# Optimization experiments

Measured on AMD Instinct MI355X. Metric: run time of the kernel, lower is better.

Reference implementation:

```python
import jax, jax.numpy as jnp
import numpy as np


def setup_inputs() -> dict:
    key = jax.random.key(0)
    k1, k2, k3, k4 = jax.random.split(key, 4)
    B, C, T, H, W = 2, 64, 8, 48, 48
    C2 = C // 2
    x_in = jax.random.normal(k1, (B, C, T, H, W), dtype=jnp.float32)
    # per-time-slice 1x1 conv weights (theta/phi pairs), kaiming-ish scale
    theta_w = jax.random.normal(k2, (T, C2, C), dtype=jnp.float32) / np.sqrt(C)
    phi_w = jax.random.normal(k3, (T, C2, C), dtype=jnp.float32) / np.sqrt(C)
    out_w = jax.random.normal(k4, (C, C), dtype=jnp.float32) / np.sqrt(C)
    return {"x_in": x_in, "theta_w": theta_w, "phi_w": phi_w, "out_w": out_w}


def reference(x_in, theta_w, phi_w, out_w):
    B, C, T, H, W = x_in.shape
    C2 = theta_w.shape[1]
    P = H * W
    # [B, T, C, P] layout: flatten spatial, move time next to batch
    x = jnp.transpose(x_in, (0, 2, 1, 3, 4)).reshape(B, T, C, P)
    # per-slice 1x1 convs == per-slice channel matmuls with slice-specific weights
    theta = jnp.einsum("toc,btcp->btop", theta_w, x)  # [B,T,C2,P]
    phi = jnp.einsum("toc,btcp->btop", phi_w, x)      # [B,T,C2,P]
    scale = 1.0 / jnp.sqrt(jnp.asarray(C2, dtype=x_in.dtype))
    scores = jnp.einsum("btcp,btcq->btpq", theta, phi) * scale  # [B,T,P,P]
    attn = jax.nn.softmax(scores, axis=-1)
    f = jnp.einsum("btpq,btcq->btcp", attn, x)  # value = raw x, [B,T,C,P]
    # conv_out: 1x1x1 Conv3d (pointwise over channels), then residual
    out = jnp.einsum("oc,btcp->btop", out_w, f)
    out = jnp.transpose(out.reshape(B, T, C, H, W), (0, 2, 1, 3, 4))
    return out + x_in
```

## Files before the change

kernel.cpp:

```cpp
#include <hip/hip_runtime.h>
#include <hip/hip_bf16.h>

#define CC 64
#define TT 8
#define PP 2304
#define C2 32
#define BT 16
#define NKT 36
#define QKT 9
#define SCALE2 0.25503486f

using h8 = __attribute__((ext_vector_type(8))) _Float16;
using h4 = __attribute__((ext_vector_type(4))) _Float16;
using f4 = __attribute__((ext_vector_type(4))) float;

#if __has_builtin(__builtin_amdgcn_exp2f)
#define EXP2(v) __builtin_amdgcn_exp2f(v)
#else
#define EXP2(v) exp2f(v)
#endif

#define SWIZ_BT(xcd, g) ((xcd) + 8 * ((g) & 1))


__global__ __launch_bounds__(256) void k_prep(
    const float* __restrict__ x, const float* __restrict__ tw,
    const float* __restrict__ pw, _Float16* __restrict__ thf,
    _Float16* __restrict__ rec) {
  const int qt = blockIdx.y >> 1, bt = SWIZ_BT(blockIdx.x, blockIdx.y);
  const int b = bt >> 3, t = bt & 7;
  const int tid = threadIdx.x;
  const int wv = tid >> 6, lane = tid & 63;
  const int quad = lane >> 4, l15 = lane & 15;

  __shared__ __align__(16) float x_s[64][68];
  __shared__ __align__(16) _Float16 th_s[4][16][32];
  __shared__ __align__(16) _Float16 ph_s[4][16][32];

  const size_t xslice = ((size_t)b * CC * TT + t) * PP;
  const int qg0 = qt * 64;

  {
    const int l16 = tid & 15;
    const int crow = tid >> 4;
#pragma unroll
    for (int ppass = 0; ppass < 4; ppass++) {
      const int c = ppass * 16 + crow;
      float4 u = *reinterpret_cast<const float4*>(
          &x[xslice + (size_t)c * (TT * PP) + qg0 + l16 * 4]);
      x_s[l16 * 4 + 0][c] = u.x;
      x_s[l16 * 4 + 1][c] = u.y;
      x_s[l16 * 4 + 2][c] = u.z;
      x_s[l16 * 4 + 3][c] = u.w;
    }
  }
  __syncthreads();

  h8 bx[2];
#pragma unroll
  for (int ks = 0; ks < 2; ks++) {
    const float* row = &x_s[wv * 16 + l15][ks * 32 + quad * 8];
    float4 u0 = *reinterpret_cast<const float4*>(row);
    float4 u1 = *reinterpret_cast<const float4*>(row + 4);
    bx[ks][0] = (_Float16)u0.x; bx[ks][1] = (_Float16)u0.y;
    bx[ks][2] = (_Float16)u0.z; bx[ks][3] = (_Float16)u0.w;
    bx[ks][4] = (_Float16)u1.x; bx[ks][5] = (_Float16)u1.y;
    bx[ks][6] = (_Float16)u1.z; bx[ks][7] = (_Float16)u1.w;
  }

  const float* twt = tw + t * C2 * CC;
  const float* pwt = pw + t * C2 * CC;
  const f4 zero = {0.f, 0.f, 0.f, 0.f};
  f4 accT[2] = {zero, zero}, accP[2] = {zero, zero};
#pragma unroll
  for (int mt = 0; mt < 2; mt++)
#pragma unroll
    for (int ks = 0; ks < 2; ks++) {
      const float* wr = twt + (mt * 16 + l15) * CC + ks * 32 + quad * 8;
      const float* pr = pwt + (mt * 16 + l15) * CC + ks * 32 + quad * 8;
      float4 a0 = *reinterpret_cast<const float4*>(wr);
      float4 a1 = *reinterpret_cast<const float4*>(wr + 4);
      float4 p0 = *reinterpret_cast<const float4*>(pr);
      float4 p1 = *reinterpret_cast<const float4*>(pr + 4);
      h8 at = {(_Float16)a0.x, (_Float16)a0.y, (_Float16)a0.z, (_Float16)a0.w,
               (_Float16)a1.x, (_Float16)a1.y, (_Float16)a1.z, (_Float16)a1.w};
      h8 ap = {(_Float16)p0.x, (_Float16)p0.y, (_Float16)p0.z, (_Float16)p0.w,
               (_Float16)p1.x, (_Float16)p1.y, (_Float16)p1.z, (_Float16)p1.w};
      accT[mt] =
          __builtin_amdgcn_mfma_f32_16x16x32_f16(at, bx[ks], accT[mt], 0, 0, 0);
      accP[mt] =
          __builtin_amdgcn_mfma_f32_16x16x32_f16(ap, bx[ks], accP[mt], 0, 0, 0);
    }

#pragma unroll
  for (int mt = 0; mt < 2; mt++) {
    h4 tv, pv;
#pragma unroll
    for (int r = 0; r < 4; r++) {
      tv[r] = (_Float16)(accT[mt][r] * SCALE2);
      pv[r] = (_Float16)accP[mt][r];
    }
    *reinterpret_cast<h4*>(&th_s[wv][l15][mt * 16 + quad * 4]) = tv;
    *reinterpret_cast<h4*>(&ph_s[wv][l15][mt * 16 + quad * 4]) = pv;
  }

  h8 tfrag = *reinterpret_cast<const h8*>(&th_s[wv][l15][quad * 8]);
  *reinterpret_cast<h8*>(
      thf + (((size_t)(bt * NKT + qt) * 4 + wv) * 64 + lane) * 8) = tfrag;

  _Float16* rb = rec + (size_t)(bt * NKT + qt) * 6144;
  h8 pfrag = *reinterpret_cast<const h8*>(&ph_s[wv][l15][quad * 8]);
  *reinterpret_cast<h8*>(rb + wv * 512 + lane * 8) = pfrag;

  {
    const int g = wv >> 1;
#pragma unroll
    for (int ct2 = 0; ct2 < 2; ct2++) {
      const int ct = (wv & 1) * 2 + ct2;
      h8 v;
#pragma unroll
      for (int j = 0; j < 4; j++) {
        v[j] = (_Float16)x_s[32 * g + quad * 4 + j][ct * 16 + l15];
        v[4 + j] = (_Float16)x_s[32 * g + 16 + quad * 4 + j][ct * 16 + l15];
      }
      *reinterpret_cast<h8*>(rb + 2048 + (g * 4 + ct) * 512 + lane * 8) = v;
    }
  }
}

__global__ __launch_bounds__(256, 3) void k_attn(
    const float* __restrict__ x, const _Float16* __restrict__ thf,
    const _Float16* __restrict__ rec, const float* __restrict__ ow,
    float* __restrict__ out) {
  const int strip = blockIdx.y >> 1;
  const int bt = SWIZ_BT(blockIdx.x, blockIdx.y);
  const int b = bt >> 3, t = bt & 7;
  const int tid = threadIdx.x;
  const int kg = tid >> 6, lane = tid & 63;
  const int quad = lane >> 4, l15 = lane & 15;

  __shared__ __align__(16) float exch[4 * 3 * 16 * 64];
  __shared__ float exl[4 * 3 * 64];

  h8 bth[3];
#pragma unroll
  for (int pf = 0; pf < 3; pf++)
    bth[pf] = *reinterpret_cast<const h8*>(
        thf + (((size_t)bt * 144 + strip * 3 + pf) * 64 + lane) * 8);

  const _Float16* recb =
      rec + ((size_t)bt * NKT + (size_t)kg * QKT) * 6144 + lane * 8;

  const f4 zero = {0.f, 0.f, 0.f, 0.f};
  f4 O[4][3];
#pragma unroll
  for (int ct = 0; ct < 4; ct++)
#pragma unroll
    for (int pf = 0; pf < 3; pf++) O[ct][pf] = zero;
  float lsum[3] = {0.f, 0.f, 0.f};

  h8 buf[12];

#pragma unroll
  for (int i = 0; i < QKT; i++) {
    const _Float16* _p = recb + (size_t)i * 6144;
#pragma unroll
    for (int j = 0; j < 12; j++)
      buf[j] = *reinterpret_cast<const h8*>(_p + j * 512);

#pragma unroll
    for (int pf = 0; pf < 3; pf++) {
      f4 s[4];
#pragma unroll
      for (int nt = 0; nt < 4; nt++)
        s[nt] = __builtin_amdgcn_mfma_f32_16x16x32_f16(buf[nt], bth[pf], zero,
                                                       0, 0, 0);
#pragma unroll
      for (int g = 0; g < 2; g++) {
        h8 bw;
#pragma unroll
        for (int r = 0; r < 4; r++) {
          float w0 = EXP2(s[2 * g][r]);
          float w1 = EXP2(s[2 * g + 1][r]);
          lsum[pf] += w0 + w1;
          bw[r] = (_Float16)w0;
          bw[4 + r] = (_Float16)w1;
        }
#pragma unroll
        for (int ct = 0; ct < 4; ct++)
          O[ct][pf] = __builtin_amdgcn_mfma_f32_16x16x32_f16(
              buf[4 + g * 4 + ct], bw, O[ct][pf], 0, 0, 0);
      }
    }
  }

#pragma unroll
  for (int pf = 0; pf < 3; pf++) {
    lsum[pf] += __shfl_xor(lsum[pf], 16);
    lsum[pf] += __shfl_xor(lsum[pf], 32);
  }

#pragma unroll
  for (int pf = 0; pf < 3; pf++) {
#pragma unroll
    for (int ct = 0; ct < 4; ct++)
#pragma unroll
      for (int r = 0; r < 4; r++)
        exch[((kg * 3 + pf) * 16 + ct * 4 + r) * 64 + lane] = O[ct][pf][r];
    exl[(kg * 3 + pf) * 64 + lane] = lsum[pf];
  }
  __syncthreads();

  if (kg < 3) {
    float ls = 0.f;
#pragma unroll
    for (int src = 0; src < 4; src++) ls += exl[(src * 3 + kg) * 64 + lane];
    const float inv = 1.f / ls;

    h4 bf[4];
#pragma unroll
    for (int ct = 0; ct < 4; ct++)
#pragma unroll
      for (int r = 0; r < 4; r++) {
        float acc = 0.f;
#pragma unroll
        for (int src = 0; src < 4; src++)
          acc += exch[((src * 3 + kg) * 16 + ct * 4 + r) * 64 + lane];
        bf[ct][r] = (_Float16)(acc * inv);
      }

    f4 D3[4] = {zero, zero, zero, zero};
#pragma unroll
    for (int mt = 0; mt < 4; mt++)
#pragma unroll
      for (int ct = 0; ct < 4; ct++) {
        const float* wrow =
            ow + (size_t)(mt * 16 + l15) * CC + ct * 16 + quad * 4;
        float4 u = *reinterpret_cast<const float4*>(wrow);
        h4 aw = {(_Float16)u.x, (_Float16)u.y, (_Float16)u.z, (_Float16)u.w};
        D3[mt] =
            __builtin_amdgcn_mfma_f32_16x16x16f16(aw, bf[ct], D3[mt], 0, 0, 0);
      }

    const int p0 = strip * 48 + kg * 16 + l15;
#pragma unroll
    for (int mt = 0; mt < 4; mt++)
#pragma unroll
      for (int r = 0; r < 4; r++) {
        const int o = mt * 16 + quad * 4 + r;
        const size_t base = ((size_t)(b * CC + o) * TT + t) * PP + p0;
        out[base] = D3[mt][r] + x[base];
      }
  }
}

extern "C" void kernel_launch(void* const* d_in, const int* in_sizes, int n_in,
                              void* d_out, int out_size, void* d_ws,
                              size_t ws_size, hipStream_t stream) {
  (void)in_sizes; (void)n_in; (void)out_size; (void)ws_size;
  const float* x = (const float*)d_in[0];
  const float* tw = (const float*)d_in[1];
  const float* pw = (const float*)d_in[2];
  const float* ow = (const float*)d_in[3];
  float* out = (float*)d_out;

  _Float16* thf = (_Float16*)d_ws;
  _Float16* rec = thf + (size_t)BT * NKT * 4 * 64 * 8;

  k_prep<<<dim3(8, 72), 256, 0, stream>>>(x, tw, pw, thf, rec);
  k_attn<<<dim3(8, 96), 256, 0, stream>>>(x, thf, rec, ow, out);
}
```

Measured before the change: 98.55 us.

## Split prep waves by role, shrink attn LDS via atomics, raise occupancy

The prep kernel now runs 512 threads: four waves compute the theta/phi projections while four others write the transposed value fragments, so the two jobs run in parallel. The attention kernel replaces its large per-wave exchange buffer with a smaller shared accumulator updated by LDS atomic adds. That cuts shared memory enough to raise the occupancy hint from 3 to 4 blocks. Score MFMAs are now issued per pair right before their exp, which lowers live registers. In exchange, the kernel adds an LDS zeroing pass, an extra barrier and atomic contention.

New measurement: 147.8 us. +50.0%, slower.

```diff
diff --git a/kernel.cpp b/kernel.cpp
--- a/kernel.cpp
+++ b/kernel.cpp
@@ -23,7 +23,7 @@
 #define SWIZ_BT(xcd, g) ((xcd) + 8 * ((g) & 1))
 
 
-__global__ __launch_bounds__(256) void k_prep(
+__global__ __launch_bounds__(512) void k_prep(
     const float* __restrict__ x, const float* __restrict__ tw,
     const float* __restrict__ pw, _Float16* __restrict__ thf,
     _Float16* __restrict__ rec) {
@@ -39,13 +39,15 @@
 
   const size_t xslice = ((size_t)b * CC * TT + t) * PP;
   const int qg0 = qt * 64;
+  _Float16* rb = rec + (size_t)(bt * NKT + qt) * 6144;
+  const f4 zero = {0.f, 0.f, 0.f, 0.f};
 
   {
     const int l16 = tid & 15;
     const int crow = tid >> 4;
 #pragma unroll
-    for (int ppass = 0; ppass < 4; ppass++) {
-      const int c = ppass * 16 + crow;
+    for (int ppass = 0; ppass < 2; ppass++) {
+      const int c = ppass * 32 + crow;
       float4 u = *reinterpret_cast<const float4*>(
           &x[xslice + (size_t)c * (TT * PP) + qg0 + l16 * 4]);
       x_s[l16 * 4 + 0][c] = u.x;
@@ -56,67 +58,68 @@
   }
   __syncthreads();
 
-  h8 bx[2];
-#pragma unroll
-  for (int ks = 0; ks < 2; ks++) {
-    const float* row = &x_s[wv * 16 + l15][ks * 32 + quad * 8];
-    float4 u0 = *reinterpret_cast<const float4*>(row);
-    float4 u1 = *reinterpret_cast<const float4*>(row + 4);
-    bx[ks][0] = (_Float16)u0.x; bx[ks][1] = (_Float16)u0.y;
-    bx[ks][2] = (_Float16)u0.z; bx[ks][3] = (_Float16)u0.w;
-    bx[ks][4] = (_Float16)u1.x; bx[ks][5] = (_Float16)u1.y;
-    bx[ks][6] = (_Float16)u1.z; bx[ks][7] = (_Float16)u1.w;
-  }
-
-  const float* twt = tw + t * C2 * CC;
-  const float* pwt = pw + t * C2 * CC;
-  const f4 zero = {0.f, 0.f, 0.f, 0.f};
-  f4 accT[2] = {zero, zero}, accP[2] = {zero, zero};
-#pragma unroll
-  for (int mt = 0; mt < 2; mt++)
+  if (wv < 4) {
+    h8 bx[2];
 #pragma unroll
     for (int ks = 0; ks < 2; ks++) {
-      const float* wr = twt + (mt * 16 + l15) * CC + ks * 32 + quad * 8;
-      const float* pr = pwt + (mt * 16 + l15) * CC + ks * 32 + quad * 8;
-      float4 a0 = *reinterpret_cast<const float4*>(wr);
-      float4 a1 = *reinterpret_cast<const float4*>(wr + 4);
-      float4 p0 = *reinterpret_cast<const float4*>(pr);
-      float4 p1 = *reinterpret_cast<const float4*>(pr + 4);
-      h8 at = {(_Float16)a0.x, (_Float16)a0.y, (_Float16)a0.z, (_Float16)a0.w,
-               (_Float16)a1.x, (_Float16)a1.y, (_Float16)a1.z, (_Float16)a1.w};
-      h8 ap = {(_Float16)p0.x, (_Float16)p0.y, (_Float16)p0.z, (_Float16)p0.w,
-               (_Float16)p1.x, (_Float16)p1.y, (_Float16)p1.z, (_Float16)p1.w};
-      accT[mt] =
-          __builtin_amdgcn_mfma_f32_16x16x32_f16(at, bx[ks], accT[mt], 0, 0, 0);
-      accP[mt] =
-          __builtin_amdgcn_mfma_f32_16x16x32_f16(ap, bx[ks], accP[mt], 0, 0, 0);
-    }
-
-#pragma unroll
-  for (int mt = 0; mt < 2; mt++) {
-    h4 tv, pv;
-#pragma unroll
-    for (int r = 0; r < 4; r++) {
-      tv[r] = (_Float16)(accT[mt][r] * SCALE2);
-      pv[r] = (_Float16)accP[mt][r];
-    }
-    *reinterpret_cast<h4*>(&th_s[wv][l15][mt * 16 + quad * 4]) = tv;
-    *reinterpret_cast<h4*>(&ph_s[wv][l15][mt * 16 + quad * 4]) = pv;
-  }
-
-  h8 tfrag = *reinterpret_cast<const h8*>(&th_s[wv][l15][quad * 8]);
-  *reinterpret_cast<h8*>(
-      thf + (((size_t)(bt * NKT + qt) * 4 + wv) * 64 + lane) * 8) = tfrag;
-
-  _Float16* rb = rec + (size_t)(bt * NKT + qt) * 6144;
-  h8 pfrag = *reinterpret_cast<const h8*>(&ph_s[wv][l15][quad * 8]);
-  *reinterpret_cast<h8*>(rb + wv * 512 + lane * 8) = pfrag;
-
-  {
-    const int g = wv >> 1;
+      const float* row = &x_s[wv * 16 + l15][ks * 32 + quad * 8];
+      float4 u0 = *reinterpret_cast<const float4*>(row);
+      float4 u1 = *reinterpret_cast<const float4*>(row + 4);
+      bx[ks][0] = (_Float16)u0.x; bx[ks][1] = (_Float16)u0.y;
+      bx[ks][2] = (_Float16)u0.z; bx[ks][3] = (_Float16)u0.w;
+      bx[ks][4] = (_Float16)u1.x; bx[ks][5] = (_Float16)u1.y;
+      bx[ks][6] = (_Float16)u1.z; bx[ks][7] = (_Float16)u1.w;
+    }
+
+    const float* twt = tw + t * C2 * CC;
+    const float* pwt = pw + t * C2 * CC;
+    f4 accT[2] = {zero, zero}, accP[2] = {zero, zero};
+#pragma unroll
+    for (int mt = 0; mt < 2; mt++)
+#pragma unroll
+      for (int ks = 0; ks < 2; ks++) {
+        const float* wr = twt + (mt * 16 + l15) * CC + ks * 32 + quad * 8;
+        const float* pr = pwt + (mt * 16 + l15) * CC + ks * 32 + quad * 8;
+        float4 a0 = *reinterpret_cast<const float4*>(wr);
+        float4 a1 = *reinterpret_cast<const float4*>(wr + 4);
+        float4 p0 = *reinterpret_cast<const float4*>(pr);
+        float4 p1 = *reinterpret_cast<const float4*>(pr + 4);
+        h8 at = {(_Float16)a0.x, (_Float16)a0.y, (_Float16)a0.z,
+                 (_Float16)a0.w, (_Float16)a1.x, (_Float16)a1.y,
+                 (_Float16)a1.z, (_Float16)a1.w};
+        h8 ap = {(_Float16)p0.x, (_Float16)p0.y, (_Float16)p0.z,
+                 (_Float16)p0.w, (_Float16)p1.x, (_Float16)p1.y,
+                 (_Float16)p1.z, (_Float16)p1.w};
+        accT[mt] = __builtin_amdgcn_mfma_f32_16x16x32_f16(at, bx[ks],
+                                                          accT[mt], 0, 0, 0);
+        accP[mt] = __builtin_amdgcn_mfma_f32_16x16x32_f16(ap, bx[ks],
+                                                          accP[mt], 0, 0, 0);
+      }
+
+#pragma unroll
+    for (int mt = 0; mt < 2; mt++) {
+      h4 tv, pv;
+#pragma unroll
+      for (int r = 0; r < 4; r++) {
+        tv[r] = (_Float16)(accT[mt][r] * SCALE2);
+        pv[r] = (_Float16)accP[mt][r];
+      }
+      *reinterpret_cast<h4*>(&th_s[wv][l15][mt * 16 + quad * 4]) = tv;
+      *reinterpret_cast<h4*>(&ph_s[wv][l15][mt * 16 + quad * 4]) = pv;
+    }
+
+    h8 tfrag = *reinterpret_cast<const h8*>(&th_s[wv][l15][quad * 8]);
+    *reinterpret_cast<h8*>(
+        thf + (((size_t)(bt * NKT + qt) * 4 + wv) * 64 + lane) * 8) = tfrag;
+
+    h8 pfrag = *reinterpret_cast<const h8*>(&ph_s[wv][l15][quad * 8]);
+    *reinterpret_cast<h8*>(rb + wv * 512 + lane * 8) = pfrag;
+  } else {
+    const int w2 = wv - 4;
+    const int g = w2 >> 1;
 #pragma unroll
     for (int ct2 = 0; ct2 < 2; ct2++) {
-      const int ct = (wv & 1) * 2 + ct2;
+      const int ct = (w2 & 1) * 2 + ct2;
       h8 v;
 #pragma unroll
       for (int j = 0; j < 4; j++) {
@@ -128,7 +131,7 @@
   }
 }
 
-__global__ __launch_bounds__(256, 3) void k_attn(
+__global__ __launch_bounds__(256, 4) void k_attn(
     const float* __restrict__ x, const _Float16* __restrict__ thf,
     const _Float16* __restrict__ rec, const float* __restrict__ ow,
     float* __restrict__ out) {
@@ -139,8 +142,15 @@
   const int kg = tid >> 6, lane = tid & 63;
   const int quad = lane >> 4, l15 = lane & 15;
 
-  __shared__ __align__(16) float exch[4 * 3 * 16 * 64];
-  __shared__ float exl[4 * 3 * 64];
+  __shared__ __align__(16) float accO[3][16][64];
+  __shared__ float accL[3][16];
+
+  {
+    float* a = &accO[0][0][0];
+    for (int i = tid; i < 3 * 16 * 64; i += 256) a[i] = 0.f;
+    if (tid < 48) (&accL[0][0])[tid] = 0.f;
+  }
+  __syncthreads();
 
   h8 bth[3];
 #pragma unroll
@@ -170,18 +180,17 @@
 
 #pragma unroll
     for (int pf = 0; pf < 3; pf++) {
-      f4 s[4];
-#pragma unroll
-      for (int nt = 0; nt < 4; nt++)
-        s[nt] = __builtin_amdgcn_mfma_f32_16x16x32_f16(buf[nt], bth[pf], zero,
-                                                       0, 0, 0);
 #pragma unroll
       for (int g = 0; g < 2; g++) {
+        f4 sA = __builtin_amdgcn_mfma_f32_16x16x32_f16(buf[2 * g], bth[pf],
+                                                       zero, 0, 0, 0);
+        f4 sB = __builtin_amdgcn_mfma_f32_16x16x32_f16(buf[2 * g + 1], bth[pf],
+                                                       zero, 0, 0, 0);
         h8 bw;
 #pragma unroll
         for (int r = 0; r < 4; r++) {
-          float w0 = EXP2(s[2 * g][r]);
-          float w1 = EXP2(s[2 * g + 1][r]);
+          float w0 = EXP2(sA[r]);
+          float w1 = EXP2(sB[r]);
           lsum[pf] += w0 + w1;
           bw[r] = (_Float16)w0;
           bw[4 + r] = (_Float16)w1;
@@ -206,28 +215,23 @@
     for (int ct = 0; ct < 4; ct++)
 #pragma unroll
       for (int r = 0; r < 4; r++)
-        exch[((kg * 3 + pf) * 16 + ct * 4 + r) * 64 + lane] = O[ct][pf][r];
-    exl[(kg * 3 + pf) * 64 + lane] = lsum[pf];
+        atomicAdd(&accO[pf][ct * 4 + r][lane], O[ct][pf][r]);
+  }
+  if (quad == 0) {
+#pragma unroll
+    for (int pf = 0; pf < 3; pf++) atomicAdd(&accL[pf][l15], lsum[pf]);
   }
   __syncthreads();
 
   if (kg < 3) {
-    float ls = 0.f;
-#pragma unroll
-    for (int src = 0; src < 4; src++) ls += exl[(src * 3 + kg) * 64 + lane];
-    const float inv = 1.f / ls;
+    const float inv = 1.f / accL[kg][l15];
 
     h4 bf[4];
 #pragma unroll
     for (int ct = 0; ct < 4; ct++)
 #pragma unroll
-      for (int r = 0; r < 4; r++) {
-        float acc = 0.f;
-#pragma unroll
-        for (int src = 0; src < 4; src++)
-          acc += exch[((src * 3 + kg) * 16 + ct * 4 + r) * 64 + lane];
-        bf[ct][r] = (_Float16)(acc * inv);
-      }
+      for (int r = 0; r < 4; r++)
+        bf[ct][r] = (_Float16)(accO[kg][ct * 4 + r][lane] * inv);
 
     f4 D3[4] = {zero, zero, zero, zero};
 #pragma unroll
@@ -267,6 +271,6 @@
   _Float16* thf = (_Float16*)d_ws;
   _Float16* rec = thf + (size_t)BT * NKT * 4 * 64 * 8;
 
-  k_prep<<<dim3(8, 72), 256, 0, stream>>>(x, tw, pw, thf, rec);
+  k_prep<<<dim3(8, 72), 512, 0, stream>>>(x, tw, pw, thf, rec);
   k_attn<<<dim3(8, 96), 256, 0, stream>>>(x, thf, rec, ow, out);
 }
```
